# Optimization experiments

Measured on AMD Instinct MI355X. Metric: run time of the kernel, lower is better.

## Reference

```python
import jax, jax.numpy as jnp
import numpy as np

VOCAB, DIM, SEQ, DEPTH, WS, MULT = 32, 256, 8192, 6, 512, 4
BATCH = 2
NEG = -1e9  # mask fill value


def setup_inputs():
    key = jax.random.key(0)
    ks = jax.random.split(key, 8)
    L, d, h = DEPTH, DIM, DIM * MULT
    s = 0.02
    return {
        "tokens": jax.random.randint(ks[0], (BATCH, SEQ), 0, VOCAB),
        "embed": jax.random.normal(ks[1], (VOCAB, d)) * s,
        "ff_ln_s": jnp.ones((L, d)),
        "ff_ln_b": jnp.zeros((L, d)),
        "w1": jax.random.normal(ks[2], (L, d, h)) * s,
        "b1": jnp.zeros((L, h)),
        "w2": jax.random.normal(ks[3], (L, h, d)) * s,
        "b2": jnp.zeros((L, d)),
        "lnf_s": jnp.ones((d,)),
        "lnf_b": jnp.zeros((d,)),
        "w_out": jax.random.normal(ks[4], (d, VOCAB)) * s,
        "b_out": jnp.zeros((VOCAB,)),
    }


def layer_norm(x, s, b, eps=1e-5):
    m = jnp.mean(x, axis=-1, keepdims=True)
    v = jnp.var(x, axis=-1, keepdims=True)
    return (x - m) * jax.lax.rsqrt(v + eps) * s + b


def rotate_half(x):
    x1, x2 = jnp.split(x, 2, axis=-1)
    return jnp.concatenate([-x2, x1], axis=-1)


def local_attn(x, ws):
    # lucidrains LocalAttention: causal, look_backward=1, look_forward=0,
    # exact_windowsize=True, rotary pos emb on q/k. q = k = v = x (no projections).
    b, n, d = x.shape
    inv_freq = 1.0 / (10000.0 ** (jnp.arange(0, d, 2, dtype=jnp.float32) / d))
    t = jnp.arange(n, dtype=jnp.float32)
    fr = t[:, None] * inv_freq[None, :]
    fr = jnp.concatenate([fr, fr], axis=-1)  # (n, d)
    qk = x * jnp.cos(fr) + rotate_half(x) * jnp.sin(fr)  # rotary applied to q and k (identical)
    w = n // ws
    bq = qk.reshape(b, w, ws, d)
    bk = bq  # q == k here
    bv = x.reshape(b, w, ws, d)
    # look_around: each window sees [previous window, current window]
    pk = jnp.pad(bk, ((0, 0), (1, 0), (0, 0), (0, 0)))[:, :-1]
    pv = jnp.pad(bv, ((0, 0), (1, 0), (0, 0), (0, 0)))[:, :-1]
    bk2 = jnp.concatenate([pk, bk], axis=2)  # (b, w, 2*ws, d)
    bv2 = jnp.concatenate([pv, bv], axis=2)
    tq = jnp.arange(n).reshape(w, ws)
    tp = jnp.pad(tq, ((1, 0), (0, 0)), constant_values=-1)[:-1]
    tk = jnp.concatenate([tp, tq], axis=1)  # (w, 2*ws), -1 marks pad
    allowed = (
        (tk[:, None, :] >= 0)
        & (tq[:, :, None] >= tk[:, None, :])          # causal
        & (tq[:, :, None] <= tk[:, None, :] + ws)     # exact windowsize (look_backward=1)
    )
    sim = jnp.einsum("bwid,bwjd->bwij", bq, bk2) * (d ** -0.5)
    sim = jnp.where(allowed[None], sim, NEG)
    attn = jax.nn.softmax(sim, axis=-1)
    out = jnp.einsum("bwij,bwjd->bwid", attn, bv2)
    return out.reshape(b, n, d)


def reference(tokens, embed, ff_ln_s, ff_ln_b, w1, b1, w2, b2, lnf_s, lnf_b, w_out, b_out):
    x = embed[tokens]  # (b, n, d)
    for i in range(DEPTH):
        x = x + local_attn(x, WS)
        h = layer_norm(x, ff_ln_s[i], ff_ln_b[i])
        h = jax.nn.gelu(h @ w1[i] + b1[i], approximate=False)
        x = x + (h @ w2[i] + b2[i])
    return layer_norm(x, lnf_s, lnf_b) @ w_out + b_out  # (b, n, vocab)
```

## Files before the change

kernel.cpp:

```cpp
#include <hip/hip_runtime.h>
#include <hip/hip_bf16.h>
#include <math.h>

#define BATCH 2
#define SEQL 8192
#define DD 256
#define HDIM 1024
#define NLAYER 6
#define WSZ 512
#define NVOCAB 32
#define PLN (DD*HDIM)

typedef unsigned short u16;
typedef __attribute__((ext_vector_type(8))) short bf16x8;
typedef __attribute__((ext_vector_type(4))) float f32x4;

union B8 { uint4 u; bf16x8 b; ushort s[8]; uint w[4]; };

__device__ inline float bf2f(u16 v){
  unsigned int u = ((unsigned int)v) << 16;
  return __uint_as_float(u);
}
__device__ inline u16 f2bf(float f){
  unsigned int u = __float_as_uint(f);
  u += 0x7fff + ((u >> 16) & 1);
  return (u16)(u >> 16);
}

__device__ __forceinline__ void gload16(const void* g, void* l){
  __builtin_amdgcn_global_load_lds(
      (const __attribute__((address_space(1))) unsigned int*)g,
      (__attribute__((address_space(3))) unsigned int*)l, 16, 0, 0);
}

__global__ void k_tables(float* __restrict__ ct, float* __restrict__ st){
  int idx = blockIdx.x * 256 + threadIdx.x;
  if (idx >= SEQL * 128) return;
  int t = idx >> 7, i = idx & 127;
  float freq = expf(-((float)i / 128.0f) * 9.210340371976184f);
  float fr = (float)t * freq;
  ct[idx] = cosf(fr);
  st[idx] = sinf(fr);
}

__global__ void k_embed(const int* __restrict__ tokens, const float* __restrict__ emb,
                        float* __restrict__ x){
  int idx = blockIdx.x * 256 + threadIdx.x;
  int bt = idx >> 6, dv = (idx & 63) << 2;
  int tok = tokens[bt];
  *(float4*)(x + bt * DD + dv) = *(const float4*)(emb + tok * DD + dv);
}

__global__ void k_rope(const float* __restrict__ x, const float* __restrict__ ct,
                       const float* __restrict__ st, u16* __restrict__ qk,
                       u16* __restrict__ xv){
  int idx = blockIdx.x * 256 + threadIdx.x;
  int bt = idx >> 5, iv = (idx & 31) << 2;
  int t = bt & (SEQL - 1);
  const float* xr = x + bt * DD;
  float4 x1 = *(const float4*)(xr + iv);
  float4 x2 = *(const float4*)(xr + 128 + iv);
  float4 c = *(const float4*)(ct + t * 128 + iv);
  float4 s = *(const float4*)(st + t * 128 + iv);
  ushort4 q1, q2, v1, v2;
  q1.x = f2bf(x1.x * c.x - x2.x * s.x);  q2.x = f2bf(x2.x * c.x + x1.x * s.x);
  q1.y = f2bf(x1.y * c.y - x2.y * s.y);  q2.y = f2bf(x2.y * c.y + x1.y * s.y);
  q1.z = f2bf(x1.z * c.z - x2.z * s.z);  q2.z = f2bf(x2.z * c.z + x1.z * s.z);
  q1.w = f2bf(x1.w * c.w - x2.w * s.w);  q2.w = f2bf(x2.w * c.w + x1.w * s.w);
  v1.x = f2bf(x1.x); v1.y = f2bf(x1.y); v1.z = f2bf(x1.z); v1.w = f2bf(x1.w);
  v2.x = f2bf(x2.x); v2.y = f2bf(x2.y); v2.z = f2bf(x2.z); v2.w = f2bf(x2.w);
  *(ushort4*)(qk + bt * DD + iv)       = q1;
  *(ushort4*)(qk + bt * DD + 128 + iv) = q2;
  *(ushort4*)(xv + bt * DD + iv)       = v1;
  *(ushort4*)(xv + bt * DD + 128 + iv) = v2;
}

__global__ void __launch_bounds__(256, 2) k_attn2(const u16* __restrict__ qk,
                                                  const u16* __restrict__ xv,
                                                  const float* __restrict__ x,
                                                  float* __restrict__ y){
  __shared__ char smem[65536];
  u16* Klds = (u16*)smem;
  u16* Vlds = (u16*)(smem + 32768);
  float* redbuf = (float*)smem;

  const int tid = threadIdx.x;
  const int lane = tid & 63;
  const int w = tid >> 6;
  const int qh = w >> 1, kh = w & 1;
  const int l15 = lane & 15, lg = lane >> 4;

  const int qb = blockIdx.x * 32;
  const int t0 = qb & (SEQL - 1);
  const size_t bbase = (size_t)(qb >> 13) << 13;

  uint4 qf[8];
  {
    const u16* qr = qk + (size_t)(qb + qh*16 + l15) * DD + lg*4;
    #pragma unroll
    for (int s = 0; s < 8; ++s){
      uint2 a = *(const uint2*)(qr + s*32);
      uint2 b = *(const uint2*)(qr + s*32 + 16);
      qf[s] = make_uint4(a.x, a.y, b.x, b.y);
    }
  }

  f32x4 oacc[16];
  #pragma unroll
  for (int d = 0; d < 16; ++d) oacc[d] = (f32x4){0.f, 0.f, 0.f, 0.f};
  float lacc = 0.f;

  const int p0 = (t0 >= WSZ) ? (t0 - WSZ) : 0;
  const int ntile = ((t0 - p0) >> 6) + 1;

  const int sk15 = tid & 15, skt = (tid >> 4) & 3, sc = tid >> 6;
  const int sdh = tid & 31, skg = tid >> 5;

  uint4 kreg[8];
  uint  vreg[2][4][4];

  {
    const u16* sb = qk + (bbase + (size_t)p0 + skt*16 + sk15) * DD;
    #pragma unroll
    for (int u = 0; u < 8; ++u) kreg[u] = *(const uint4*)(sb + u*32 + sc*8);
    #pragma unroll
    for (int kg = 0; kg < 2; ++kg){
      int sk0 = (skg + kg*8) * 4;
      #pragma unroll
      for (int u = 0; u < 4; ++u){
        int d0 = sdh*2 + u*64;
        const u16* vb = xv + (bbase + (size_t)p0 + sk0) * DD + d0;
        vreg[kg][u][0] = *(const uint*)(vb);
        vreg[kg][u][1] = *(const uint*)(vb + DD);
        vreg[kg][u][2] = *(const uint*)(vb + 2*DD);
        vreg[kg][u][3] = *(const uint*)(vb + 3*DD);
      }
    }
  }
  #pragma unroll
  for (int u = 0; u < 8; ++u){
    int d0 = u*32 + sc*8;
    int s = d0 >> 5, r = d0 & 31;
    int h = r >> 4, lgw = (r & 15) >> 2;
    int rec = ((s*4 + skt)*4 + lgw)*16 + sk15;
    char* wp = (char*)Klds + rec*16 + h*8;
    *(uint2*)wp         = make_uint2(kreg[u].x, kreg[u].y);
    *(uint2*)(wp + 256) = make_uint2(kreg[u].z, kreg[u].w);
  }
  #pragma unroll
  for (int kg = 0; kg < 2; ++kg){
    int sk0 = (skg + kg*8) * 4;
    int vkhw = sk0 >> 5, vh = (sk0 >> 4) & 1, vlgw = (sk0 >> 2) & 3;
    #pragma unroll
    for (int u = 0; u < 4; ++u){
      int d0 = sdh*2 + u*64;
      uint a0 = vreg[kg][u][0], a1 = vreg[kg][u][1], a2 = vreg[kg][u][2], a3 = vreg[kg][u][3];
      uint w0 = (a0 & 0xffffu) | (a1 << 16);
      uint w1 = (a2 & 0xffffu) | (a3 << 16);
      uint w2 = (a0 >> 16) | (a1 & 0xffff0000u);
      uint w3 = (a2 >> 16) | (a3 & 0xffff0000u);
      int dimt = d0 >> 4, d15 = d0 & 15;
      int rec = ((dimt*2 + vkhw)*4 + vlgw)*16 + d15;
      char* wp = (char*)Vlds + rec*16 + vh*8;
      *(uint2*)wp        = make_uint2(w0, w1);
      *(uint2*)(wp + 16) = make_uint2(w2, w3);
    }
  }
  __syncthreads();

  for (int ti = 0; ti < ntile; ++ti){
    const int p = p0 + ti*64;
    if (ti + 1 < ntile){
      const int pn = p + 64;
      const u16* sb = qk + (bbase + (size_t)pn + skt*16 + sk15) * DD;
      #pragma unroll
      for (int u = 0; u < 8; ++u) kreg[u] = *(const uint4*)(sb + u*32 + sc*8);
      #pragma unroll
      for (int kg = 0; kg < 2; ++kg){
        int sk0 = (skg + kg*8) * 4;
        #pragma unroll
        for (int u = 0; u < 4; ++u){
          int d0 = sdh*2 + u*64;
          const u16* vb = xv + (bbase + (size_t)pn + sk0) * DD + d0;
          vreg[kg][u][0] = *(const uint*)(vb);
          vreg[kg][u][1] = *(const uint*)(vb + DD);
          vreg[kg][u][2] = *(const uint*)(vb + 2*DD);
          vreg[kg][u][3] = *(const uint*)(vb + 3*DD);
        }
      }
    }

    f32x4 sacc[2];
    sacc[0] = (f32x4){0.f,0.f,0.f,0.f};
    sacc[1] = (f32x4){0.f,0.f,0.f,0.f};
    #pragma unroll
    for (int s = 0; s < 8; ++s){
      B8 ka0, ka1, qbf;
      ka0.b = *(const bf16x8*)((char*)Klds + (((s*4 + kh*2+0)*4 + lg)*16 + l15)*16);
      ka1.b = *(const bf16x8*)((char*)Klds + (((s*4 + kh*2+1)*4 + lg)*16 + l15)*16);
      qbf.u = qf[s];
      sacc[0] = __builtin_amdgcn_mfma_f32_16x16x32_bf16(ka0.b, qbf.b, sacc[0], 0, 0, 0);
      sacc[1] = __builtin_amdgcn_mfma_f32_16x16x32_bf16(ka1.b, qbf.b, sacc[1], 0, 0, 0);
    }

    B8 pa;
    #pragma unroll
    for (int ktp = 0; ktp < 2; ++ktp){
      int kbase = p + kh*32 + ktp*16 + lg*4;
      int qpos = t0 + qh*16 + l15;
      #pragma unroll
      for (int r = 0; r < 4; ++r){
        int kpos = kbase + r;
        float sv = sacc[ktp][r] * 0.0625f;
        bool ok = (kpos <= qpos) && (qpos <= kpos + WSZ);
        float pv = ok ? __expf(sv) : 0.0f;
        lacc += pv;
        pa.s[ktp*4 + r] = f2bf(pv);
      }
    }

    #pragma unroll
    for (int dimt = 0; dimt < 16; ++dimt){
      B8 vb;
      vb.b = *(const bf16x8*)((char*)Vlds + (((dimt*2 + kh)*4 + lg)*16 + l15)*16);
      oacc[dimt] = __builtin_amdgcn_mfma_f32_16x16x32_bf16(pa.b, vb.b, oacc[dimt], 0, 0, 0);
    }

    __syncthreads();
    if (ti + 1 < ntile){
      #pragma unroll
      for (int u = 0; u < 8; ++u){
        int d0 = u*32 + sc*8;
        int s = d0 >> 5, r = d0 & 31;
        int h = r >> 4, lgw = (r & 15) >> 2;
        int rec = ((s*4 + skt)*4 + lgw)*16 + sk15;
        char* wp = (char*)Klds + rec*16 + h*8;
        *(uint2*)wp         = make_uint2(kreg[u].x, kreg[u].y);
        *(uint2*)(wp + 256) = make_uint2(kreg[u].z, kreg[u].w);
      }
      #pragma unroll
      for (int kg = 0; kg < 2; ++kg){
        int sk0 = (skg + kg*8) * 4;
        int vkhw = sk0 >> 5, vh = (sk0 >> 4) & 1, vlgw = (sk0 >> 2) & 3;
        #pragma unroll
        for (int u = 0; u < 4; ++u){
          int d0 = sdh*2 + u*64;
          uint a0 = vreg[kg][u][0], a1 = vreg[kg][u][1], a2 = vreg[kg][u][2], a3 = vreg[kg][u][3];
          uint w0 = (a0 & 0xffffu) | (a1 << 16);
          uint w1 = (a2 & 0xffffu) | (a3 << 16);
          uint w2 = (a0 >> 16) | (a1 & 0xffff0000u);
          uint w3 = (a2 >> 16) | (a3 & 0xffff0000u);
          int dimt = d0 >> 4, d15 = d0 & 15;
          int rec = ((dimt*2 + vkhw)*4 + vlgw)*16 + d15;
          char* wp = (char*)Vlds + rec*16 + vh*8;
          *(uint2*)wp        = make_uint2(w0, w1);
          *(uint2*)(wp + 16) = make_uint2(w2, w3);
        }
      }
    }
    __syncthreads();
  }

  lacc += __shfl_xor(lacc, 16, 64);
  lacc += __shfl_xor(lacc, 32, 64);
  if (lane < 16) redbuf[kh*32 + qh*16 + l15] = lacc;
  __syncthreads();
  if (tid < 32) redbuf[64 + tid] = redbuf[tid] + redbuf[32 + tid];
  __syncthreads();

  float* opass = redbuf + 96;
  #pragma unroll
  for (int pass = 0; pass < 8; ++pass){
    #pragma unroll
    for (int dt = 0; dt < 2; ++dt){
      int dimt = pass*2 + dt;
      #pragma unroll
      for (int r = 0; r < 4; ++r){
        int qrow = qh*16 + lg*4 + r;
        opass[(kh*32 + qrow)*36 + dt*16 + l15] = oacc[dimt][r];
      }
    }
    __syncthreads();
    {
      int q = tid >> 3, dv = (tid & 7) * 4;
      float4 o0 = *(float4*)&opass[q*36 + dv];
      float4 o1 = *(float4*)&opass[(32 + q)*36 + dv];
      float inv = 1.0f / redbuf[64 + q];
      size_t gi = (size_t)(qb + q) * DD + pass*32 + dv;
      float4 xr = *(const float4*)(x + gi);
      float4 ov;
      ov.x = xr.x + (o0.x + o1.x) * inv;
      ov.y = xr.y + (o0.y + o1.y) * inv;
      ov.z = xr.z + (o0.z + o1.z) * inv;
      ov.w = xr.w + (o0.w + o1.w) * inv;
      *(float4*)(y + gi) = ov;
    }
    __syncthreads();
  }
}

__global__ void __launch_bounds__(256) k_ln(const float* __restrict__ in,
                                            const float* __restrict__ g,
                                            const float* __restrict__ b,
                                            u16* __restrict__ out){
  int wid = (blockIdx.x * 256 + threadIdx.x) >> 6;
  int lane = threadIdx.x & 63;
  float4 v = *(const float4*)(in + wid * DD + lane * 4);
  float s = v.x + v.y + v.z + v.w;
  float ss = v.x * v.x + v.y * v.y + v.z * v.z + v.w * v.w;
  #pragma unroll
  for (int o = 32; o; o >>= 1){ s += __shfl_xor(s, o, 64); ss += __shfl_xor(ss, o, 64); }
  float m = s * (1.0f / DD);
  float var = ss * (1.0f / DD) - m * m;
  float rs = rsqrtf(var + 1e-5f);
  float4 gf = *(const float4*)(g + lane * 4);
  float4 bf = *(const float4*)(b + lane * 4);
  ushort4 o4;
  o4.x = f2bf((v.x - m) * rs * gf.x + bf.x);
  o4.y = f2bf((v.y - m) * rs * gf.y + bf.y);
  o4.z = f2bf((v.z - m) * rs * gf.z + bf.z);
  o4.w = f2bf((v.w - m) * rs * gf.w + bf.w);
  *(ushort4*)(out + wid * DD + lane * 4) = o4;
}

template<int KDIM, int NDIM>
__device__ __forceinline__ void split_one(const float* __restrict__ W,
                                          u16* __restrict__ Phi,
                                          u16* __restrict__ Plo, int idx){
  int c15 = idx & 15;
  int lg = (idx >> 4) & 3;
  int nt = (idx >> 6) % (NDIM/16);
  int ks = idx / ((NDIM/16) * 64);
  int col = nt*16 + c15;
  B8 hi, lo;
  #pragma unroll
  for (int j = 0; j < 8; ++j){
    int k = ks*32 + (j >> 2)*16 + lg*4 + (j & 3);
    float wv = W[(size_t)k * NDIM + col];
    u16 hv = f2bf(wv);
    hi.s[j] = hv;
    lo.s[j] = f2bf(wv - bf2f(hv));
  }
  *(uint4*)(Phi + (size_t)idx * 8) = hi.u;
  *(uint4*)(Plo + (size_t)idx * 8) = lo.u;
}

__global__ void __launch_bounds__(256) k_split2(const float* __restrict__ W1,
                                                const float* __restrict__ W2,
                                                u16* __restrict__ P){
  int b = blockIdx.x;
  if (b < 128) split_one<DD, HDIM>(W1, P, P + PLN, b*256 + threadIdx.x);
  else         split_one<HDIM, DD>(W2, P + 2*PLN, P + 3*PLN, (b - 128)*256 + threadIdx.x);
}

template<int KDIM, int NDIM, int EPI>
__global__ void __launch_bounds__(256) k_gemm(const u16* __restrict__ A,
                                              const u16* __restrict__ BhG,
                                              const u16* __restrict__ BlG,
                                              const float* __restrict__ bias,
                                              const float* __restrict__ res,
                                              float* __restrict__ outf,
                                              u16* __restrict__ outh){
  __shared__ char smem[18432 + 16384];
  char* As = smem;
  char* Bs = smem + 18432;

  const int tid = threadIdx.x;
  const int lane = tid & 63;
  const int w = tid >> 6;
  const int wr = w >> 1, wc = w & 1;
  const int l15 = lane & 15, lg = lane >> 4;
  const int m0 = blockIdx.y * 128;
  const int n0 = blockIdx.x * 64;
  const int NT16 = NDIM / 16;

  f32x4 acc[4][2];
  #pragma unroll
  for (int a = 0; a < 4; ++a){
    acc[a][0] = (f32x4){0.f,0.f,0.f,0.f};
    acc[a][1] = (f32x4){0.f,0.f,0.f,0.f};
  }

  for (int kb = 0; kb < KDIM/64; ++kb){
    __syncthreads();
    #pragma unroll
    for (int p = 0; p < 4; ++p){
      int c = p*256 + tid;
      int row = c >> 3, cc = c & 7;
      uint4 v = *(const uint4*)(A + (size_t)(m0 + row) * KDIM + kb*64 + cc*8);
      *(uint4*)(As + row*144 + cc*16) = v;
    }
    #pragma unroll
    for (int p = 0; p < 4; ++p){
      int j = p*256 + tid;
      int plane = j >> 9, rem = j & 511;
      int chunk = rem >> 6, r = rem & 63;
      const u16* src = (plane ? BlG : BhG)
          + (((size_t)(kb*2 + (chunk >> 2)) * NT16 + (n0 >> 4) + (chunk & 3))*64 + r)*8;
      gload16(src, Bs + j*16);
    }
    __syncthreads();

    #pragma unroll
    for (int s = 0; s < 2; ++s){
      B8 af[4], bhf[2], blf[2];
      #pragma unroll
      for (int a = 0; a < 4; ++a){
        const char* ab = As + (wr*64 + a*16 + l15)*144 + s*64 + lg*8;
        uint2 lo = *(const uint2*)ab;
        uint2 hi = *(const uint2*)(ab + 32);
        af[a].u = make_uint4(lo.x, lo.y, hi.x, hi.y);
      }
      #pragma unroll
      for (int c = 0; c < 2; ++c){
        int off = (((s*4 + wc*2 + c)*64) + lg*16 + l15)*16;
        bhf[c].u = *(const uint4*)(Bs + off);
        blf[c].u = *(const uint4*)(Bs + 8192 + off);
      }
      #pragma unroll
      for (int a = 0; a < 4; ++a)
        #pragma unroll
        for (int c = 0; c < 2; ++c){
          acc[a][c] = __builtin_amdgcn_mfma_f32_16x16x32_bf16(af[a].b, bhf[c].b, acc[a][c], 0, 0, 0);
          acc[a][c] = __builtin_amdgcn_mfma_f32_16x16x32_bf16(af[a].b, blf[c].b, acc[a][c], 0, 0, 0);
        }
    }
  }

  float bv[2];
  bv[0] = bias[n0 + wc*32 + l15];
  bv[1] = bias[n0 + wc*32 + 16 + l15];

  #pragma unroll
  for (int a = 0; a < 4; ++a){
    #pragma unroll
    for (int c = 0; c < 2; ++c){
      #pragma unroll
      for (int r = 0; r < 4; ++r){
        int row = m0 + wr*64 + a*16 + lg*4 + r;
        int col = n0 + wc*32 + c*16 + l15;
        float v = acc[a][c][r] + bv[c];
        if (EPI == 0){
          float gl = 0.5f * v * (1.0f + erff(v * 0.70710678f));
          outh[(size_t)row * NDIM + col] = f2bf(gl);
        } else {
          outf[(size_t)row * NDIM + col] = v + res[(size_t)row * NDIM + col];
        }
      }
    }
  }
}

__global__ void __launch_bounds__(256) k_final(const float* __restrict__ x,
                                               const float* __restrict__ g,
                                               const float* __restrict__ b,
                                               const float* __restrict__ wout,
                                               const float* __restrict__ bout,
                                               float* __restrict__ out){
  __shared__ float lds[4][256];
  int widx = threadIdx.x >> 6, lane = threadIdx.x & 63;
  int bt = blockIdx.x * 4 + widx;
  float4 v = *(const float4*)(x + bt * DD + lane * 4);
  float s = v.x + v.y + v.z + v.w;
  float ss = v.x * v.x + v.y * v.y + v.z * v.z + v.w * v.w;
  #pragma unroll
  for (int o = 32; o; o >>= 1){ s += __shfl_xor(s, o, 64); ss += __shfl_xor(ss, o, 64); }
  float m = s * (1.0f / DD);
  float var = ss * (1.0f / DD) - m * m;
  float rs = rsqrtf(var + 1e-5f);
  float4 gf = *(const float4*)(g + lane * 4);
  float4 bf = *(const float4*)(b + lane * 4);
  lds[widx][lane * 4 + 0] = (v.x - m) * rs * gf.x + bf.x;
  lds[widx][lane * 4 + 1] = (v.y - m) * rs * gf.y + bf.y;
  lds[widx][lane * 4 + 2] = (v.z - m) * rs * gf.z + bf.z;
  lds[widx][lane * 4 + 3] = (v.w - m) * rs * gf.w + bf.w;
  __syncthreads();
  int vo = lane & 31, half = lane >> 5;
  const float* lp = &lds[widx][half * 128];
  const float* wp = wout + half * 128 * NVOCAB + vo;
  float acc = 0;
  #pragma unroll 4
  for (int d = 0; d < 128; ++d) acc += lp[d] * wp[d * NVOCAB];
  acc += __shfl_down(acc, 32, 64);
  if (lane < 32) out[bt * NVOCAB + vo] = acc + bout[vo];
}

extern "C" void kernel_launch(void* const* d_in, const int* in_sizes, int n_in,
                              void* d_out, int out_size, void* d_ws, size_t ws_size,
                              hipStream_t stream) {
  const int*   tokens = (const int*)d_in[0];
  const float* emb   = (const float*)d_in[1];
  const float* ffs   = (const float*)d_in[2];
  const float* ffb   = (const float*)d_in[3];
  const float* w1    = (const float*)d_in[4];
  const float* b1    = (const float*)d_in[5];
  const float* w2    = (const float*)d_in[6];
  const float* b2    = (const float*)d_in[7];
  const float* lnfs  = (const float*)d_in[8];
  const float* lnfb  = (const float*)d_in[9];
  const float* wout  = (const float*)d_in[10];
  const float* bout  = (const float*)d_in[11];
  float* out = (float*)d_out;

  char* ws = (char*)d_ws;
  float* x    = (float*)(ws);
  float* y    = (float*)(ws + (size_t)16*1024*1024);
  u16*   buf8 = (u16*)  (ws + (size_t)32*1024*1024);
  u16*   qk   = (u16*)  (ws + (size_t)40*1024*1024);
  u16*   h    = (u16*)  (ws + (size_t)48*1024*1024);
  float* ct   = (float*)(ws + (size_t)80*1024*1024);
  float* st   = (float*)(ws + (size_t)84*1024*1024);

  k_tables<<<4096, 256, 0, stream>>>(ct, st);
  k_embed<<<4096, 256, 0, stream>>>(tokens, emb, x);
  for (int L = 0; L < NLAYER; ++L){
    k_rope<<<2048, 256, 0, stream>>>(x, ct, st, qk, buf8);
    k_attn2<<<512, 256, 0, stream>>>(qk, buf8, x, y);
    k_ln  <<<4096, 256, 0, stream>>>(y, ffs + L*DD, ffb + L*DD, buf8);
    k_split2<<<256, 256, 0, stream>>>(w1 + (size_t)L*PLN, w2 + (size_t)L*PLN, qk);
    k_gemm<DD, HDIM, 0><<<dim3(16, 128), 256, 0, stream>>>(
        buf8, qk, qk + PLN, b1 + L*HDIM, nullptr, nullptr, h);
    k_gemm<HDIM, DD, 1><<<dim3(4, 128), 256, 0, stream>>>(
        h, qk + 2*PLN, qk + 3*PLN, b2 + L*DD, y, x, nullptr);
  }
  k_final<<<4096, 256, 0, stream>>>(x, lnfs, lnfb, wout, bout, out);
}
```

Before: 817.4 us.

## Transpose V in rope kernel and read K/V directly from global in attention

Result: slower. 1.284 ms (+57.1%).

```diff
diff --git a/kernel.cpp b/kernel.cpp
--- a/kernel.cpp
+++ b/kernel.cpp
@@ -51,52 +51,63 @@
   *(float4*)(x + bt * DD + dv) = *(const float4*)(emb + tok * DD + dv);
 }
 
-__global__ void k_rope(const float* __restrict__ x, const float* __restrict__ ct,
-                       const float* __restrict__ st, u16* __restrict__ qk,
-                       u16* __restrict__ xv){
-  int idx = blockIdx.x * 256 + threadIdx.x;
-  int bt = idx >> 5, iv = (idx & 31) << 2;
-  int t = bt & (SEQL - 1);
-  const float* xr = x + bt * DD;
-  float4 x1 = *(const float4*)(xr + iv);
-  float4 x2 = *(const float4*)(xr + 128 + iv);
-  float4 c = *(const float4*)(ct + t * 128 + iv);
-  float4 s = *(const float4*)(st + t * 128 + iv);
-  ushort4 q1, q2, v1, v2;
-  q1.x = f2bf(x1.x * c.x - x2.x * s.x);  q2.x = f2bf(x2.x * c.x + x1.x * s.x);
-  q1.y = f2bf(x1.y * c.y - x2.y * s.y);  q2.y = f2bf(x2.y * c.y + x1.y * s.y);
-  q1.z = f2bf(x1.z * c.z - x2.z * s.z);  q2.z = f2bf(x2.z * c.z + x1.z * s.z);
-  q1.w = f2bf(x1.w * c.w - x2.w * s.w);  q2.w = f2bf(x2.w * c.w + x1.w * s.w);
-  v1.x = f2bf(x1.x); v1.y = f2bf(x1.y); v1.z = f2bf(x1.z); v1.w = f2bf(x1.w);
-  v2.x = f2bf(x2.x); v2.y = f2bf(x2.y); v2.z = f2bf(x2.z); v2.w = f2bf(x2.w);
-  *(ushort4*)(qk + bt * DD + iv)       = q1;
-  *(ushort4*)(qk + bt * DD + 128 + iv) = q2;
-  *(ushort4*)(xv + bt * DD + iv)       = v1;
-  *(ushort4*)(xv + bt * DD + 128 + iv) = v2;
-}
-
-__global__ void __launch_bounds__(256, 2) k_attn2(const u16* __restrict__ qk,
-                                                  const u16* __restrict__ xv,
-                                                  const float* __restrict__ x,
-                                                  float* __restrict__ y){
-  __shared__ char smem[65536];
-  u16* Klds = (u16*)smem;
-  u16* Vlds = (u16*)(smem + 32768);
-  float* redbuf = (float*)smem;
-
+__global__ void __launch_bounds__(256) k_rope2(const float* __restrict__ x,
+                                               const float* __restrict__ ct,
+                                               const float* __restrict__ st,
+                                               u16* __restrict__ qk,
+                                               u16* __restrict__ xvT){
+  __shared__ u16 vt[256][66];
+  const int tid = threadIdx.x;
+  const int tok0 = blockIdx.x * 64;
+
+  #pragma unroll
+  for (int u = 0; u < 32; ++u){
+    int e = u*256 + tid;
+    int tok = e >> 7, i = e & 127;
+    int row = tok0 + tok;
+    int t = row & (SEQL - 1);
+    float x1 = x[(size_t)row*DD + i];
+    float x2 = x[(size_t)row*DD + 128 + i];
+    float c = ct[t*128 + i], s = st[t*128 + i];
+    qk[(size_t)row*DD + i]       = f2bf(x1*c - x2*s);
+    qk[(size_t)row*DD + 128 + i] = f2bf(x2*c + x1*s);
+    vt[i][tok]       = f2bf(x1);
+    vt[i + 128][tok] = f2bf(x2);
+  }
+  __syncthreads();
+
+  const int batch = tok0 >> 13;
+  const int tloc = tok0 & (SEQL - 1);
+  #pragma unroll
+  for (int u = 0; u < 8; ++u){
+    int j = u*256 + tid;
+    int dim = j >> 3, tg = j & 7;
+    B8 pk;
+    #pragma unroll
+    for (int e = 0; e < 8; ++e) pk.s[e] = vt[dim][tg*8 + e];
+    *(uint4*)(xvT + ((size_t)batch*DD + dim)*SEQL + tloc + tg*8) = pk.u;
+  }
+}
+
+__global__ void __launch_bounds__(256) k_attn3(const u16* __restrict__ qk,
+                                               const u16* __restrict__ xvT,
+                                               const float* __restrict__ x,
+                                               float* __restrict__ y){
+  __shared__ float Obuf[16][258];
+  __shared__ float Lbuf[64];
   const int tid = threadIdx.x;
   const int lane = tid & 63;
-  const int w = tid >> 6;
-  const int qh = w >> 1, kh = w & 1;
+  const int myw = tid >> 6;
   const int l15 = lane & 15, lg = lane >> 4;
 
-  const int qb = blockIdx.x * 32;
+  const int qb = blockIdx.x * 16;
   const int t0 = qb & (SEQL - 1);
-  const size_t bbase = (size_t)(qb >> 13) << 13;
+  const int batch = qb >> 13;
+  const size_t kbb = (size_t)batch << 13;
 
   uint4 qf[8];
   {
-    const u16* qr = qk + (size_t)(qb + qh*16 + l15) * DD + lg*4;
+    const u16* qr = qk + (size_t)(qb + l15)*DD + lg*4;
     #pragma unroll
     for (int s = 0; s < 8; ++s){
       uint2 a = *(const uint2*)(qr + s*32);
@@ -107,195 +118,105 @@
 
   f32x4 oacc[16];
   #pragma unroll
-  for (int d = 0; d < 16; ++d) oacc[d] = (f32x4){0.f, 0.f, 0.f, 0.f};
+  for (int d = 0; d < 16; ++d) oacc[d] = (f32x4){0.f,0.f,0.f,0.f};
   float lacc = 0.f;
 
-  const int p0 = (t0 >= WSZ) ? (t0 - WSZ) : 0;
-  const int ntile = ((t0 - p0) >> 6) + 1;
-
-  const int sk15 = tid & 15, skt = (tid >> 4) & 3, sc = tid >> 6;
-  const int sdh = tid & 31, skg = tid >> 5;
-
-  uint4 kreg[8];
-  uint  vreg[2][4][4];
-
-  {
-    const u16* sb = qk + (bbase + (size_t)p0 + skt*16 + sk15) * DD;
-    #pragma unroll
-    for (int u = 0; u < 8; ++u) kreg[u] = *(const uint4*)(sb + u*32 + sc*8);
-    #pragma unroll
-    for (int kg = 0; kg < 2; ++kg){
-      int sk0 = (skg + kg*8) * 4;
-      #pragma unroll
-      for (int u = 0; u < 4; ++u){
-        int d0 = sdh*2 + u*64;
-        const u16* vb = xv + (bbase + (size_t)p0 + sk0) * DD + d0;
-        vreg[kg][u][0] = *(const uint*)(vb);
-        vreg[kg][u][1] = *(const uint*)(vb + DD);
-        vreg[kg][u][2] = *(const uint*)(vb + 2*DD);
-        vreg[kg][u][3] = *(const uint*)(vb + 3*DD);
-      }
-    }
-  }
-  #pragma unroll
-  for (int u = 0; u < 8; ++u){
-    int d0 = u*32 + sc*8;
-    int s = d0 >> 5, r = d0 & 31;
-    int h = r >> 4, lgw = (r & 15) >> 2;
-    int rec = ((s*4 + skt)*4 + lgw)*16 + sk15;
-    char* wp = (char*)Klds + rec*16 + h*8;
-    *(uint2*)wp         = make_uint2(kreg[u].x, kreg[u].y);
-    *(uint2*)(wp + 256) = make_uint2(kreg[u].z, kreg[u].w);
-  }
-  #pragma unroll
-  for (int kg = 0; kg < 2; ++kg){
-    int sk0 = (skg + kg*8) * 4;
-    int vkhw = sk0 >> 5, vh = (sk0 >> 4) & 1, vlgw = (sk0 >> 2) & 3;
-    #pragma unroll
-    for (int u = 0; u < 4; ++u){
-      int d0 = sdh*2 + u*64;
-      uint a0 = vreg[kg][u][0], a1 = vreg[kg][u][1], a2 = vreg[kg][u][2], a3 = vreg[kg][u][3];
-      uint w0 = (a0 & 0xffffu) | (a1 << 16);
-      uint w1 = (a2 & 0xffffu) | (a3 << 16);
-      uint w2 = (a0 >> 16) | (a1 & 0xffff0000u);
-      uint w3 = (a2 >> 16) | (a3 & 0xffff0000u);
-      int dimt = d0 >> 4, d15 = d0 & 15;
-      int rec = ((dimt*2 + vkhw)*4 + vlgw)*16 + d15;
-      char* wp = (char*)Vlds + rec*16 + vh*8;
-      *(uint2*)wp        = make_uint2(w0, w1);
-      *(uint2*)(wp + 16) = make_uint2(w2, w3);
-    }
-  }
-  __syncthreads();
-
-  for (int ti = 0; ti < ntile; ++ti){
-    const int p = p0 + ti*64;
-    if (ti + 1 < ntile){
-      const int pn = p + 64;
-      const u16* sb = qk + (bbase + (size_t)pn + skt*16 + sk15) * DD;
-      #pragma unroll
-      for (int u = 0; u < 8; ++u) kreg[u] = *(const uint4*)(sb + u*32 + sc*8);
-      #pragma unroll
-      for (int kg = 0; kg < 2; ++kg){
-        int sk0 = (skg + kg*8) * 4;
-        #pragma unroll
-        for (int u = 0; u < 4; ++u){
-          int d0 = sdh*2 + u*64;
-          const u16* vb = xv + (bbase + (size_t)pn + sk0) * DD + d0;
-          vreg[kg][u][0] = *(const uint*)(vb);
-          vreg[kg][u][1] = *(const uint*)(vb + DD);
-          vreg[kg][u][2] = *(const uint*)(vb + 2*DD);
-          vreg[kg][u][3] = *(const uint*)(vb + 3*DD);
-        }
-      }
-    }
-
+  const int pstart = (t0 >= WSZ) ? ((t0 - WSZ) & ~31) : 0;
+  const int nt = ((t0 + 15 - pstart) >> 5) + 1;
+  const int qpos = t0 + l15;
+
+  for (int ti = myw; ti < nt; ti += 4){
+    const int p = pstart + ti*32;
     f32x4 sacc[2];
     sacc[0] = (f32x4){0.f,0.f,0.f,0.f};
     sacc[1] = (f32x4){0.f,0.f,0.f,0.f};
     #pragma unroll
-    for (int s = 0; s < 8; ++s){
-      B8 ka0, ka1, qbf;
-      ka0.b = *(const bf16x8*)((char*)Klds + (((s*4 + kh*2+0)*4 + lg)*16 + l15)*16);
-      ka1.b = *(const bf16x8*)((char*)Klds + (((s*4 + kh*2+1)*4 + lg)*16 + l15)*16);
-      qbf.u = qf[s];
-      sacc[0] = __builtin_amdgcn_mfma_f32_16x16x32_bf16(ka0.b, qbf.b, sacc[0], 0, 0, 0);
-      sacc[1] = __builtin_amdgcn_mfma_f32_16x16x32_bf16(ka1.b, qbf.b, sacc[1], 0, 0, 0);
-    }
-
+    for (int ktp = 0; ktp < 2; ++ktp){
+      int kp0 = p + ktp*16;
+      if (kp0 > t0 + 15) continue;
+      if (kp0 + 15 < t0 - WSZ) continue;
+      const u16* kr = qk + (kbb + kp0 + l15)*DD + lg*4;
+      #pragma unroll
+      for (int s = 0; s < 8; ++s){
+        uint2 a = *(const uint2*)(kr + s*32);
+        uint2 b = *(const uint2*)(kr + s*32 + 16);
+        B8 ka; ka.u = make_uint4(a.x, a.y, b.x, b.y);
+        B8 qbf; qbf.u = qf[s];
+        sacc[ktp] = __builtin_amdgcn_mfma_f32_16x16x32_bf16(ka.b, qbf.b, sacc[ktp], 0, 0, 0);
+      }
+    }
     B8 pa;
     #pragma unroll
-    for (int ktp = 0; ktp < 2; ++ktp){
-      int kbase = p + kh*32 + ktp*16 + lg*4;
-      int qpos = t0 + qh*16 + l15;
-      #pragma unroll
-      for (int r = 0; r < 4; ++r){
-        int kpos = kbase + r;
-        float sv = sacc[ktp][r] * 0.0625f;
-        bool ok = (kpos <= qpos) && (qpos <= kpos + WSZ);
-        float pv = ok ? __expf(sv) : 0.0f;
-        lacc += pv;
-        pa.s[ktp*4 + r] = f2bf(pv);
-      }
-    }
-
+    for (int j = 0; j < 8; ++j){
+      int ktp = j >> 2, r = j & 3;
+      int kpos = p + ktp*16 + lg*4 + r;
+      float sv = sacc[ktp][r] * 0.0625f;
+      bool ok = (kpos <= qpos) && (qpos <= kpos + WSZ);
+      float pv = ok ? __expf(sv) : 0.0f;
+      lacc += pv;
+      pa.s[j] = f2bf(pv);
+    }
     #pragma unroll
     for (int dimt = 0; dimt < 16; ++dimt){
-      B8 vb;
-      vb.b = *(const bf16x8*)((char*)Vlds + (((dimt*2 + kh)*4 + lg)*16 + l15)*16);
+      const u16* vr = xvT + ((size_t)(batch*DD + dimt*16 + l15))*SEQL + p + lg*4;
+      uint2 a = *(const uint2*)vr;
+      uint2 b = *(const uint2*)(vr + 16);
+      B8 vb; vb.u = make_uint4(a.x, a.y, b.x, b.y);
       oacc[dimt] = __builtin_amdgcn_mfma_f32_16x16x32_bf16(pa.b, vb.b, oacc[dimt], 0, 0, 0);
     }
-
-    __syncthreads();
-    if (ti + 1 < ntile){
-      #pragma unroll
-      for (int u = 0; u < 8; ++u){
-        int d0 = u*32 + sc*8;
-        int s = d0 >> 5, r = d0 & 31;
-        int h = r >> 4, lgw = (r & 15) >> 2;
-        int rec = ((s*4 + skt)*4 + lgw)*16 + sk15;
-        char* wp = (char*)Klds + rec*16 + h*8;
-        *(uint2*)wp         = make_uint2(kreg[u].x, kreg[u].y);
-        *(uint2*)(wp + 256) = make_uint2(kreg[u].z, kreg[u].w);
-      }
-      #pragma unroll
-      for (int kg = 0; kg < 2; ++kg){
-        int sk0 = (skg + kg*8) * 4;
-        int vkhw = sk0 >> 5, vh = (sk0 >> 4) & 1, vlgw = (sk0 >> 2) & 3;
-        #pragma unroll
-        for (int u = 0; u < 4; ++u){
-          int d0 = sdh*2 + u*64;
-          uint a0 = vreg[kg][u][0], a1 = vreg[kg][u][1], a2 = vreg[kg][u][2], a3 = vreg[kg][u][3];
-          uint w0 = (a0 & 0xffffu) | (a1 << 16);
-          uint w1 = (a2 & 0xffffu) | (a3 << 16);
-          uint w2 = (a0 >> 16) | (a1 & 0xffff0000u);
-          uint w3 = (a2 >> 16) | (a3 & 0xffff0000u);
-          int dimt = d0 >> 4, d15 = d0 & 15;
-          int rec = ((dimt*2 + vkhw)*4 + vlgw)*16 + d15;
-          char* wp = (char*)Vlds + rec*16 + vh*8;
-          *(uint2*)wp        = make_uint2(w0, w1);
-          *(uint2*)(wp + 16) = make_uint2(w2, w3);
-        }
-      }
-    }
-    __syncthreads();
   }
 
   lacc += __shfl_xor(lacc, 16, 64);
   lacc += __shfl_xor(lacc, 32, 64);
-  if (lane < 16) redbuf[kh*32 + qh*16 + l15] = lacc;
-  __syncthreads();
-  if (tid < 32) redbuf[64 + tid] = redbuf[tid] + redbuf[32 + tid];
-  __syncthreads();
-
-  float* opass = redbuf + 96;
-  #pragma unroll
-  for (int pass = 0; pass < 8; ++pass){
-    #pragma unroll
-    for (int dt = 0; dt < 2; ++dt){
-      int dimt = pass*2 + dt;
-      #pragma unroll
-      for (int r = 0; r < 4; ++r){
-        int qrow = qh*16 + lg*4 + r;
-        opass[(kh*32 + qrow)*36 + dt*16 + l15] = oacc[dimt][r];
-      }
-    }
-    __syncthreads();
-    {
-      int q = tid >> 3, dv = (tid & 7) * 4;
-      float4 o0 = *(float4*)&opass[q*36 + dv];
-      float4 o1 = *(float4*)&opass[(32 + q)*36 + dv];
-      float inv = 1.0f / redbuf[64 + q];
-      size_t gi = (size_t)(qb + q) * DD + pass*32 + dv;
-      float4 xr = *(const float4*)(x + gi);
-      float4 ov;
-      ov.x = xr.x + (o0.x + o1.x) * inv;
-      ov.y = xr.y + (o0.y + o1.y) * inv;
-      ov.z = xr.z + (o0.z + o1.z) * inv;
-      ov.w = xr.w + (o0.w + o1.w) * inv;
-      *(float4*)(y + gi) = ov;
-    }
-    __syncthreads();
+  if (lane < 16) Lbuf[myw*16 + lane] = lacc;
+  __syncthreads();
+  if (myw == 0){
+    #pragma unroll
+    for (int dimt = 0; dimt < 16; ++dimt)
+      #pragma unroll
+      for (int r = 0; r < 4; ++r)
+        Obuf[lg*4 + r][dimt*16 + l15] = oacc[dimt][r];
+  }
+  __syncthreads();
+  if (myw == 1){
+    #pragma unroll
+    for (int dimt = 0; dimt < 16; ++dimt)
+      #pragma unroll
+      for (int r = 0; r < 4; ++r)
+        Obuf[lg*4 + r][dimt*16 + l15] += oacc[dimt][r];
+  }
+  __syncthreads();
+  if (myw == 2){
+    #pragma unroll
+    for (int dimt = 0; dimt < 16; ++dimt)
+      #pragma unroll
+      for (int r = 0; r < 4; ++r)
+        Obuf[lg*4 + r][dimt*16 + l15] += oacc[dimt][r];
+  }
+  __syncthreads();
+  if (myw == 3){
+    #pragma unroll
+    for (int dimt = 0; dimt < 16; ++dimt)
+      #pragma unroll
+      for (int r = 0; r < 4; ++r)
+        Obuf[lg*4 + r][dimt*16 + l15] += oacc[dimt][r];
+  }
+  __syncthreads();
+
+  #pragma unroll
+  for (int u = 0; u < 4; ++u){
+    int task = u*256 + tid;
+    int q = task >> 6, dv = (task & 63) * 4;
+    float lt = Lbuf[q] + Lbuf[16 + q] + Lbuf[32 + q] + Lbuf[48 + q];
+    float inv = 1.0f / lt;
+    size_t gi = (size_t)(qb + q)*DD + dv;
+    float4 xr = *(const float4*)(x + gi);
+    float4 ov;
+    ov.x = xr.x + Obuf[q][dv + 0] * inv;
+    ov.y = xr.y + Obuf[q][dv + 1] * inv;
+    ov.z = xr.z + Obuf[q][dv + 2] * inv;
+    ov.w = xr.w + Obuf[q][dv + 3] * inv;
+    *(float4*)(y + gi) = ov;
   }
 }
 
@@ -505,21 +426,22 @@
   char* ws = (char*)d_ws;
   float* x    = (float*)(ws);
   float* y    = (float*)(ws + (size_t)16*1024*1024);
-  u16*   buf8 = (u16*)  (ws + (size_t)32*1024*1024);
+  u16*   xvT  = (u16*)  (ws + (size_t)32*1024*1024);
   u16*   qk   = (u16*)  (ws + (size_t)40*1024*1024);
   u16*   h    = (u16*)  (ws + (size_t)48*1024*1024);
   float* ct   = (float*)(ws + (size_t)80*1024*1024);
   float* st   = (float*)(ws + (size_t)84*1024*1024);
+  u16* lnx = xvT;
 
   k_tables<<<4096, 256, 0, stream>>>(ct, st);
   k_embed<<<4096, 256, 0, stream>>>(tokens, emb, x);
   for (int L = 0; L < NLAYER; ++L){
-    k_rope<<<2048, 256, 0, stream>>>(x, ct, st, qk, buf8);
-    k_attn2<<<512, 256, 0, stream>>>(qk, buf8, x, y);
-    k_ln  <<<4096, 256, 0, stream>>>(y, ffs + L*DD, ffb + L*DD, buf8);
+    k_rope2<<<256, 256, 0, stream>>>(x, ct, st, qk, xvT);
+    k_attn3<<<1024, 256, 0, stream>>>(qk, xvT, x, y);
+    k_ln  <<<4096, 256, 0, stream>>>(y, ffs + L*DD, ffb + L*DD, lnx);
     k_split2<<<256, 256, 0, stream>>>(w1 + (size_t)L*PLN, w2 + (size_t)L*PLN, qk);
     k_gemm<DD, HDIM, 0><<<dim3(16, 128), 256, 0, stream>>>(
-        buf8, qk, qk + PLN, b1 + L*HDIM, nullptr, nullptr, h);
+        lnx, qk, qk + PLN, b1 + L*HDIM, nullptr, nullptr, h);
     k_gemm<HDIM, DD, 1><<<dim3(4, 128), 256, 0, stream>>>(
         h, qk + 2*PLN, qk + 3*PLN, b2 + L*DD, y, x, nullptr);
   }
```

## Split attention key tiles across block pairs with 64-query blocks and fused combine+LN

Applied to the files above, without the earlier changes.

Result: no change. 816.3 us (-0.1%).

```diff
diff --git a/kernel.cpp b/kernel.cpp
--- a/kernel.cpp
+++ b/kernel.cpp
@@ -9,6 +9,7 @@
 #define NLAYER 6
 #define WSZ 512
 #define NVOCAB 32
+#define NTOK (BATCH*SEQL)
 #define PLN (DD*HDIM)
 
 typedef unsigned short u16;
@@ -75,10 +76,10 @@
   *(ushort4*)(xv + bt * DD + 128 + iv) = v2;
 }
 
-__global__ void __launch_bounds__(256, 2) k_attn2(const u16* __restrict__ qk,
+__global__ void __launch_bounds__(512, 2) k_attn4(const u16* __restrict__ qk,
                                                   const u16* __restrict__ xv,
-                                                  const float* __restrict__ x,
-                                                  float* __restrict__ y){
+                                                  u16* __restrict__ Opart,
+                                                  float* __restrict__ lpart){
   __shared__ char smem[65536];
   u16* Klds = (u16*)smem;
   u16* Vlds = (u16*)(smem + 32768);
@@ -90,7 +91,9 @@
   const int qh = w >> 1, kh = w & 1;
   const int l15 = lane & 15, lg = lane >> 4;
 
-  const int qb = blockIdx.x * 32;
+  const int qg = blockIdx.x >> 1;
+  const int half = blockIdx.x & 1;
+  const int qb = qg * 64;
   const int t0 = qb & (SEQL - 1);
   const size_t bbase = (size_t)(qb >> 13) << 13;
 
@@ -112,49 +115,46 @@
 
   const int p0 = (t0 >= WSZ) ? (t0 - WSZ) : 0;
   const int ntile = ((t0 - p0) >> 6) + 1;
+  const int nt2 = ntile >> 1;
+  const int tstart = half ? nt2 : 0;
+  const int tend   = half ? ntile : nt2;
 
   const int sk15 = tid & 15, skt = (tid >> 4) & 3, sc = tid >> 6;
-  const int sdh = tid & 31, skg = tid >> 5;
-
-  uint4 kreg[8];
-  uint  vreg[2][4][4];
-
-  {
-    const u16* sb = qk + (bbase + (size_t)p0 + skt*16 + sk15) * DD;
-    #pragma unroll
-    for (int u = 0; u < 8; ++u) kreg[u] = *(const uint4*)(sb + u*32 + sc*8);
-    #pragma unroll
-    for (int kg = 0; kg < 2; ++kg){
-      int sk0 = (skg + kg*8) * 4;
+  const int sdh = tid & 31, sk0 = (tid >> 5) * 4;
+  const int vkhw = sk0 >> 5, vh = (sk0 >> 4) & 1, vlgw = (sk0 >> 2) & 3;
+
+  if (tstart < tend){
+    uint4 kreg[4];
+    uint  vreg[4][4];
+    const int pfirst = p0 + tstart*64;
+    {
+      const u16* sb = qk + (bbase + (size_t)pfirst + skt*16 + sk15) * DD;
+      #pragma unroll
+      for (int u = 0; u < 4; ++u) kreg[u] = *(const uint4*)(sb + u*64 + sc*8);
       #pragma unroll
       for (int u = 0; u < 4; ++u){
         int d0 = sdh*2 + u*64;
-        const u16* vb = xv + (bbase + (size_t)p0 + sk0) * DD + d0;
-        vreg[kg][u][0] = *(const uint*)(vb);
-        vreg[kg][u][1] = *(const uint*)(vb + DD);
-        vreg[kg][u][2] = *(const uint*)(vb + 2*DD);
-        vreg[kg][u][3] = *(const uint*)(vb + 3*DD);
-      }
-    }
-  }
-  #pragma unroll
-  for (int u = 0; u < 8; ++u){
-    int d0 = u*32 + sc*8;
-    int s = d0 >> 5, r = d0 & 31;
-    int h = r >> 4, lgw = (r & 15) >> 2;
-    int rec = ((s*4 + skt)*4 + lgw)*16 + sk15;
-    char* wp = (char*)Klds + rec*16 + h*8;
-    *(uint2*)wp         = make_uint2(kreg[u].x, kreg[u].y);
-    *(uint2*)(wp + 256) = make_uint2(kreg[u].z, kreg[u].w);
-  }
-  #pragma unroll
-  for (int kg = 0; kg < 2; ++kg){
-    int sk0 = (skg + kg*8) * 4;
-    int vkhw = sk0 >> 5, vh = (sk0 >> 4) & 1, vlgw = (sk0 >> 2) & 3;
+        const u16* vb = xv + (bbase + (size_t)pfirst + sk0) * DD + d0;
+        vreg[u][0] = *(const uint*)(vb);
+        vreg[u][1] = *(const uint*)(vb + DD);
+        vreg[u][2] = *(const uint*)(vb + 2*DD);
+        vreg[u][3] = *(const uint*)(vb + 3*DD);
+      }
+    }
+    #pragma unroll
+    for (int u = 0; u < 4; ++u){
+      int d0 = u*64 + sc*8;
+      int s = d0 >> 5, r = d0 & 31;
+      int h = r >> 4, lgw = (r & 15) >> 2;
+      int rec = ((s*4 + skt)*4 + lgw)*16 + sk15;
+      char* wp = (char*)Klds + rec*16 + h*8;
+      *(uint2*)wp         = make_uint2(kreg[u].x, kreg[u].y);
+      *(uint2*)(wp + 256) = make_uint2(kreg[u].z, kreg[u].w);
+    }
     #pragma unroll
     for (int u = 0; u < 4; ++u){
       int d0 = sdh*2 + u*64;
-      uint a0 = vreg[kg][u][0], a1 = vreg[kg][u][1], a2 = vreg[kg][u][2], a3 = vreg[kg][u][3];
+      uint a0 = vreg[u][0], a1 = vreg[u][1], a2 = vreg[u][2], a3 = vreg[u][3];
       uint w0 = (a0 & 0xffffu) | (a1 << 16);
       uint w1 = (a2 & 0xffffu) | (a3 << 16);
       uint w2 = (a0 >> 16) | (a1 & 0xffff0000u);
@@ -165,87 +165,78 @@
       *(uint2*)wp        = make_uint2(w0, w1);
       *(uint2*)(wp + 16) = make_uint2(w2, w3);
     }
-  }
-  __syncthreads();
-
-  for (int ti = 0; ti < ntile; ++ti){
-    const int p = p0 + ti*64;
-    if (ti + 1 < ntile){
-      const int pn = p + 64;
-      const u16* sb = qk + (bbase + (size_t)pn + skt*16 + sk15) * DD;
-      #pragma unroll
-      for (int u = 0; u < 8; ++u) kreg[u] = *(const uint4*)(sb + u*32 + sc*8);
-      #pragma unroll
-      for (int kg = 0; kg < 2; ++kg){
-        int sk0 = (skg + kg*8) * 4;
+    __syncthreads();
+
+    for (int ti = tstart; ti < tend; ++ti){
+      const int p = p0 + ti*64;
+      if (ti + 1 < tend){
+        const int pn = p + 64;
+        const u16* sb = qk + (bbase + (size_t)pn + skt*16 + sk15) * DD;
+        #pragma unroll
+        for (int u = 0; u < 4; ++u) kreg[u] = *(const uint4*)(sb + u*64 + sc*8);
         #pragma unroll
         for (int u = 0; u < 4; ++u){
           int d0 = sdh*2 + u*64;
           const u16* vb = xv + (bbase + (size_t)pn + sk0) * DD + d0;
-          vreg[kg][u][0] = *(const uint*)(vb);
-          vreg[kg][u][1] = *(const uint*)(vb + DD);
-          vreg[kg][u][2] = *(const uint*)(vb + 2*DD);
-          vreg[kg][u][3] = *(const uint*)(vb + 3*DD);
+          vreg[u][0] = *(const uint*)(vb);
+          vreg[u][1] = *(const uint*)(vb + DD);
+          vreg[u][2] = *(const uint*)(vb + 2*DD);
+          vreg[u][3] = *(const uint*)(vb + 3*DD);
         }
       }
-    }
-
-    f32x4 sacc[2];
-    sacc[0] = (f32x4){0.f,0.f,0.f,0.f};
-    sacc[1] = (f32x4){0.f,0.f,0.f,0.f};
-    #pragma unroll
-    for (int s = 0; s < 8; ++s){
-      B8 ka0, ka1, qbf;
-      ka0.b = *(const bf16x8*)((char*)Klds + (((s*4 + kh*2+0)*4 + lg)*16 + l15)*16);
-      ka1.b = *(const bf16x8*)((char*)Klds + (((s*4 + kh*2+1)*4 + lg)*16 + l15)*16);
-      qbf.u = qf[s];
-      sacc[0] = __builtin_amdgcn_mfma_f32_16x16x32_bf16(ka0.b, qbf.b, sacc[0], 0, 0, 0);
-      sacc[1] = __builtin_amdgcn_mfma_f32_16x16x32_bf16(ka1.b, qbf.b, sacc[1], 0, 0, 0);
-    }
-
-    B8 pa;
-    #pragma unroll
-    for (int ktp = 0; ktp < 2; ++ktp){
-      int kbase = p + kh*32 + ktp*16 + lg*4;
-      int qpos = t0 + qh*16 + l15;
-      #pragma unroll
-      for (int r = 0; r < 4; ++r){
-        int kpos = kbase + r;
-        float sv = sacc[ktp][r] * 0.0625f;
-        bool ok = (kpos <= qpos) && (qpos <= kpos + WSZ);
-        float pv = ok ? __expf(sv) : 0.0f;
-        lacc += pv;
-        pa.s[ktp*4 + r] = f2bf(pv);
-      }
-    }
-
-    #pragma unroll
-    for (int dimt = 0; dimt < 16; ++dimt){
-      B8 vb;
-      vb.b = *(const bf16x8*)((char*)Vlds + (((dimt*2 + kh)*4 + lg)*16 + l15)*16);
-      oacc[dimt] = __builtin_amdgcn_mfma_f32_16x16x32_bf16(pa.b, vb.b, oacc[dimt], 0, 0, 0);
-    }
-
-    __syncthreads();
-    if (ti + 1 < ntile){
-      #pragma unroll
-      for (int u = 0; u < 8; ++u){
-        int d0 = u*32 + sc*8;
-        int s = d0 >> 5, r = d0 & 31;
-        int h = r >> 4, lgw = (r & 15) >> 2;
-        int rec = ((s*4 + skt)*4 + lgw)*16 + sk15;
-        char* wp = (char*)Klds + rec*16 + h*8;
-        *(uint2*)wp         = make_uint2(kreg[u].x, kreg[u].y);
-        *(uint2*)(wp + 256) = make_uint2(kreg[u].z, kreg[u].w);
-      }
-      #pragma unroll
-      for (int kg = 0; kg < 2; ++kg){
-        int sk0 = (skg + kg*8) * 4;
-        int vkhw = sk0 >> 5, vh = (sk0 >> 4) & 1, vlgw = (sk0 >> 2) & 3;
+
+      f32x4 sacc[2];
+      sacc[0] = (f32x4){0.f,0.f,0.f,0.f};
+      sacc[1] = (f32x4){0.f,0.f,0.f,0.f};
+      #pragma unroll
+      for (int s = 0; s < 8; ++s){
+        B8 ka0, ka1, qbf;
+        ka0.b = *(const bf16x8*)((char*)Klds + (((s*4 + kh*2+0)*4 + lg)*16 + l15)*16);
+        ka1.b = *(const bf16x8*)((char*)Klds + (((s*4 + kh*2+1)*4 + lg)*16 + l15)*16);
+        qbf.u = qf[s];
+        sacc[0] = __builtin_amdgcn_mfma_f32_16x16x32_bf16(ka0.b, qbf.b, sacc[0], 0, 0, 0);
+        sacc[1] = __builtin_amdgcn_mfma_f32_16x16x32_bf16(ka1.b, qbf.b, sacc[1], 0, 0, 0);
+      }
+
+      B8 pa;
+      #pragma unroll
+      for (int ktp = 0; ktp < 2; ++ktp){
+        int kbase = p + kh*32 + ktp*16 + lg*4;
+        int qpos = t0 + qh*16 + l15;
+        #pragma unroll
+        for (int r = 0; r < 4; ++r){
+          int kpos = kbase + r;
+          float sv = sacc[ktp][r] * 0.0625f;
+          bool ok = (kpos <= qpos) && (qpos <= kpos + WSZ);
+          float pv = ok ? __expf(sv) : 0.0f;
+          lacc += pv;
+          pa.s[ktp*4 + r] = f2bf(pv);
+        }
+      }
+
+      #pragma unroll
+      for (int dimt = 0; dimt < 16; ++dimt){
+        B8 vb;
+        vb.b = *(const bf16x8*)((char*)Vlds + (((dimt*2 + kh)*4 + lg)*16 + l15)*16);
+        oacc[dimt] = __builtin_amdgcn_mfma_f32_16x16x32_bf16(pa.b, vb.b, oacc[dimt], 0, 0, 0);
+      }
+
+      __syncthreads();
+      if (ti + 1 < tend){
+        #pragma unroll
+        for (int u = 0; u < 4; ++u){
+          int d0 = u*64 + sc*8;
+          int s = d0 >> 5, r = d0 & 31;
+          int h = r >> 4, lgw = (r & 15) >> 2;
+          int rec = ((s*4 + skt)*4 + lgw)*16 + sk15;
+          char* wp = (char*)Klds + rec*16 + h*8;
+          *(uint2*)wp         = make_uint2(kreg[u].x, kreg[u].y);
+          *(uint2*)(wp + 256) = make_uint2(kreg[u].z, kreg[u].w);
+        }
         #pragma unroll
         for (int u = 0; u < 4; ++u){
           int d0 = sdh*2 + u*64;
-          uint a0 = vreg[kg][u][0], a1 = vreg[kg][u][1], a2 = vreg[kg][u][2], a3 = vreg[kg][u][3];
+          uint a0 = vreg[u][0], a1 = vreg[u][1], a2 = vreg[u][2], a3 = vreg[u][3];
           uint w0 = (a0 & 0xffffu) | (a1 << 16);
           uint w1 = (a2 & 0xffffu) | (a3 << 16);
           uint w2 = (a0 >> 16) | (a1 & 0xffff0000u);
@@ -257,18 +248,20 @@
           *(uint2*)(wp + 16) = make_uint2(w2, w3);
         }
       }
-    }
+      __syncthreads();
+    }
+  } else {
     __syncthreads();
   }
 
   lacc += __shfl_xor(lacc, 16, 64);
   lacc += __shfl_xor(lacc, 32, 64);
-  if (lane < 16) redbuf[kh*32 + qh*16 + l15] = lacc;
   __syncthreads();
-  if (tid < 32) redbuf[64 + tid] = redbuf[tid] + redbuf[32 + tid];
+  if (lane < 16) redbuf[kh*64 + qh*16 + l15] = lacc;
   __syncthreads();
-
-  float* opass = redbuf + 96;
+  if (tid < 64) lpart[(size_t)half*NTOK + qb + tid] = redbuf[tid] + redbuf[64 + tid];
+
+  float* opass = redbuf + 192;
   #pragma unroll
   for (int pass = 0; pass < 8; ++pass){
     #pragma unroll
@@ -277,50 +270,60 @@
       #pragma unroll
       for (int r = 0; r < 4; ++r){
         int qrow = qh*16 + lg*4 + r;
-        opass[(kh*32 + qrow)*36 + dt*16 + l15] = oacc[dimt][r];
+        opass[(kh*64 + qrow)*36 + dt*16 + l15] = oacc[dimt][r];
       }
     }
     __syncthreads();
     {
       int q = tid >> 3, dv = (tid & 7) * 4;
       float4 o0 = *(float4*)&opass[q*36 + dv];
-      float4 o1 = *(float4*)&opass[(32 + q)*36 + dv];
-      float inv = 1.0f / redbuf[64 + q];
-      size_t gi = (size_t)(qb + q) * DD + pass*32 + dv;
-      float4 xr = *(const float4*)(x + gi);
-      float4 ov;
-      ov.x = xr.x + (o0.x + o1.x) * inv;
-      ov.y = xr.y + (o0.y + o1.y) * inv;
-      ov.z = xr.z + (o0.z + o1.z) * inv;
-      ov.w = xr.w + (o0.w + o1.w) * inv;
-      *(float4*)(y + gi) = ov;
+      float4 o1 = *(float4*)&opass[(64 + q)*36 + dv];
+      ushort4 o4;
+      o4.x = f2bf(o0.x + o1.x);
+      o4.y = f2bf(o0.y + o1.y);
+      o4.z = f2bf(o0.z + o1.z);
+      o4.w = f2bf(o0.w + o1.w);
+      *(ushort4*)(Opart + ((size_t)half*NTOK + qb + q)*DD + pass*32 + dv) = o4;
     }
     __syncthreads();
   }
 }
 
-__global__ void __launch_bounds__(256) k_ln(const float* __restrict__ in,
-                                            const float* __restrict__ g,
-                                            const float* __restrict__ b,
-                                            u16* __restrict__ out){
+__global__ void __launch_bounds__(256) k_comb(const u16* __restrict__ Opart,
+                                              const float* __restrict__ lpart,
+                                              const float* __restrict__ x,
+                                              const float* __restrict__ g,
+                                              const float* __restrict__ b,
+                                              float* __restrict__ y,
+                                              u16* __restrict__ lnx){
   int wid = (blockIdx.x * 256 + threadIdx.x) >> 6;
   int lane = threadIdx.x & 63;
-  float4 v = *(const float4*)(in + wid * DD + lane * 4);
+  float inv = 1.0f / (lpart[wid] + lpart[NTOK + wid]);
+  ushort4 o0 = *(const ushort4*)(Opart + (size_t)wid*DD + lane*4);
+  ushort4 o1 = *(const ushort4*)(Opart + ((size_t)NTOK + wid)*DD + lane*4);
+  float4 xr = *(const float4*)(x + (size_t)wid*DD + lane*4);
+  float4 v;
+  v.x = xr.x + (bf2f(o0.x) + bf2f(o1.x)) * inv;
+  v.y = xr.y + (bf2f(o0.y) + bf2f(o1.y)) * inv;
+  v.z = xr.z + (bf2f(o0.z) + bf2f(o1.z)) * inv;
+  v.w = xr.w + (bf2f(o0.w) + bf2f(o1.w)) * inv;
+  *(float4*)(y + (size_t)wid*DD + lane*4) = v;
+
   float s = v.x + v.y + v.z + v.w;
-  float ss = v.x * v.x + v.y * v.y + v.z * v.z + v.w * v.w;
+  float ss = v.x*v.x + v.y*v.y + v.z*v.z + v.w*v.w;
   #pragma unroll
   for (int o = 32; o; o >>= 1){ s += __shfl_xor(s, o, 64); ss += __shfl_xor(ss, o, 64); }
   float m = s * (1.0f / DD);
   float var = ss * (1.0f / DD) - m * m;
   float rs = rsqrtf(var + 1e-5f);
-  float4 gf = *(const float4*)(g + lane * 4);
-  float4 bf = *(const float4*)(b + lane * 4);
+  float4 gf = *(const float4*)(g + lane*4);
+  float4 bf = *(const float4*)(b + lane*4);
   ushort4 o4;
   o4.x = f2bf((v.x - m) * rs * gf.x + bf.x);
   o4.y = f2bf((v.y - m) * rs * gf.y + bf.y);
   o4.z = f2bf((v.z - m) * rs * gf.z + bf.z);
   o4.w = f2bf((v.w - m) * rs * gf.w + bf.w);
-  *(ushort4*)(out + wid * DD + lane * 4) = o4;
+  *(ushort4*)(lnx + (size_t)wid*DD + lane*4) = o4;
 }
 
 template<int KDIM, int NDIM>
@@ -511,12 +514,15 @@
   float* ct   = (float*)(ws + (size_t)80*1024*1024);
   float* st   = (float*)(ws + (size_t)84*1024*1024);
 
+  u16*   Opart = h;
+  float* lpart = (float*)(ws + (size_t)64*1024*1024);
+
   k_tables<<<4096, 256, 0, stream>>>(ct, st);
   k_embed<<<4096, 256, 0, stream>>>(tokens, emb, x);
   for (int L = 0; L < NLAYER; ++L){
     k_rope<<<2048, 256, 0, stream>>>(x, ct, st, qk, buf8);
-    k_attn2<<<512, 256, 0, stream>>>(qk, buf8, x, y);
-    k_ln  <<<4096, 256, 0, stream>>>(y, ffs + L*DD, ffb + L*DD, buf8);
+    k_attn4<<<512, 512, 0, stream>>>(qk, buf8, Opart, lpart);
+    k_comb<<<4096, 256, 0, stream>>>(Opart, lpart, x, ffs + L*DD, ffb + L*DD, y, buf8);
     k_split2<<<256, 256, 0, stream>>>(w1 + (size_t)L*PLN, w2 + (size_t)L*PLN, qk);
     k_gemm<DD, HDIM, 0><<<dim3(16, 128), 256, 0, stream>>>(
         buf8, qk, qk + PLN, b1 + L*HDIM, nullptr, nullptr, h);
```
